# Kernel tuning notes

Measured on AMD Instinct MI355X. Metric: run time of the kernel, lower is better.

Reference implementation:

```python
import jax, jax.numpy as jnp
import numpy as np

# TT config (matches init_kwargs)
NUM_TABLES = 4
P = (100, 100, 100)          # tt_p_shapes, prod = num_embeddings = 1e6
Q = (4, 4, 4)                # tt_q_shapes, prod = embedding_dim = 64
R = (1, 32, 32, 1)           # tt_ranks with boundary ranks
BAGS_PER_TABLE = 8192
POOL = 16                    # indices per bag


def setup_inputs() -> dict:
    key = jax.random.key(0)
    k1, k2, k3, k4 = jax.random.split(key, 4)
    nnz = NUM_TABLES * BAGS_PER_TABLE * POOL      # 524288
    B = NUM_TABLES * BAGS_PER_TABLE               # 32768 bags total
    indices = jax.random.randint(k1, (nnz,), 0, P[0] * P[1] * P[2], dtype=jnp.int64)
    offsets = (jnp.arange(B + 1, dtype=jnp.int64) * POOL)
    scale = 0.05  # small init, akin to approx-normal weight_dist
    tt_core_0 = jax.random.normal(k2, (NUM_TABLES, P[0], R[0] * Q[0] * R[1]), dtype=jnp.float32) * scale
    tt_core_1 = jax.random.normal(k3, (NUM_TABLES, P[1], R[1] * Q[1] * R[2]), dtype=jnp.float32) * scale
    tt_core_2 = jax.random.normal(k4, (NUM_TABLES, P[2], R[2] * Q[2] * R[3]), dtype=jnp.float32) * scale
    return {"indices": indices, "offsets": offsets,
            "tt_core_0": tt_core_0, "tt_core_1": tt_core_1, "tt_core_2": tt_core_2}


def reference(indices, offsets, tt_core_0, tt_core_1, tt_core_2):
    nnz = indices.shape[0]
    B = offsets.shape[0] - 1
    bags_per_table = B // NUM_TABLES

    # bag id for each nonzero (embedding-bag semantics), then table id per nonzero
    rowidx = jnp.searchsorted(offsets, jnp.arange(nnz, dtype=offsets.dtype), side='right') - 1
    tableidx = rowidx // bags_per_table

    # decompose flat row index into TT indices (C-order over p-shapes,
    # matching tt_matrix_to_full row layout)
    i0 = indices // (P[1] * P[2])
    i1 = (indices // P[2]) % P[1]
    i2 = indices % P[2]

    # gather per-lookup core slices
    c0 = tt_core_0[tableidx, i0].reshape(nnz, Q[0], R[1])          # r0 == 1
    c1 = tt_core_1[tableidx, i1].reshape(nnz, R[1], Q[1], R[2])
    c2 = tt_core_2[tableidx, i2].reshape(nnz, R[2], Q[2])          # r3 == 1

    # on-the-fly TT contraction to reconstruct embedding rows [nnz, D]
    t = jnp.einsum('nar,nrbs->nabs', c0, c1)                       # [nnz, q0, q1, r2]
    rows = jnp.einsum('nabs,nsc->nabc', t, c2).reshape(nnz, Q[0] * Q[1] * Q[2])

    # sum-pool per bag
    out = jax.ops.segment_sum(rows, rowidx, num_segments=B)        # [B, D]
    return out
```

## Files before the change

### kernel.cpp

```cpp
#include <hip/hip_runtime.h>
#include <stdint.h>

#define NT 4
#define PP 100
#define TT_BYTES (4ull * 100 * 100 * 1024)
#define C2B_DWORDS (NT * PP * 64)


typedef short bf16x8 __attribute__((ext_vector_type(8)));
typedef float f32x4  __attribute__((ext_vector_type(4)));

__device__ __forceinline__ uint32_t f2bf(float f) {
    union { float f; uint32_t u; } v; v.f = f;
    uint32_t u = v.u;
    return (u + 0x7fffu + ((u >> 16) & 1u)) >> 16;
}

__global__ __launch_bounds__(256)
void tt_phase1(const float* __restrict__ c0g, const float* __restrict__ c1g,
               unsigned short* __restrict__ tT,
               const float* __restrict__ c2g, uint32_t* __restrict__ c2p) {
    __shared__ uint32_t       A_l[112 * 16];
    __shared__ uint32_t       B_l[128 * 16];
    __shared__ unsigned short D_l[100 * 128];

    int blk = blockIdx.x;
    int tid = threadIdx.x;

    if (blk >= 1600) {
        int t = (blk - 1600) * 256 + tid;
        if (t < C2B_DWORDS) {
            int sg = t & 15, c = (t >> 4) & 3, combo = t >> 6;
            const float* src = c2g + (size_t)combo * 128;
            c2p[t] = f2bf(src[(2 * sg) * 4 + c]) | (f2bf(src[(2 * sg + 1) * 4 + c]) << 16);
        }
        return;
    }

    int tab = blk / 400;
    int rem = blk % 400;
    int i1  = rem >> 2;
    int ch  = rem & 3;

    if (tid < 192) A_l[1600 + tid] = 0u;

    const float2* a2 = (const float2*)(c0g + (size_t)tab * 12800 + (size_t)ch * 3200);
    #pragma unroll
    for (int it = 0; it < 7; ++it) {
        int d = tid + it * 256;
        if (d < 1600) {
            float2 v = a2[d];
            int row = d >> 4, kd = d & 15;
            A_l[row * 16 + (kd ^ ((row & 3) << 2))] = f2bf(v.x) | (f2bf(v.y) << 16);
        }
    }
    const float* c1row = c1g + ((size_t)tab * PP + i1) * 4096;
    #pragma unroll
    for (int it = 0; it < 8; ++it) {
        int j = tid + it * 256;
        int n = j & 127, rp = j >> 7;
        float e = c1row[(2 * rp) * 128 + n];
        float o = c1row[(2 * rp + 1) * 128 + n];
        B_l[n * 16 + (rp ^ ((n & 3) << 2))] = f2bf(e) | (f2bf(o) << 16);
    }
    __syncthreads();

    int lane = tid & 63, wv = tid >> 6;
    int col = lane & 15, kq = lane >> 4;

    #pragma unroll
    for (int mt = 0; mt < 7; ++mt) {
        #pragma unroll
        for (int ntl = 0; ntl < 2; ++ntl) {
            int nt = wv * 2 + ntl;
            int arow = mt * 16 + col;
            int bn   = nt * 16 + col;
            bf16x8 af = *(const bf16x8*)&A_l[arow * 16 + ((kq ^ (arow & 3)) << 2)];
            bf16x8 bf = *(const bf16x8*)&B_l[bn   * 16 + ((kq ^ (bn   & 3)) << 2)];
            f32x4 acc = {0.f, 0.f, 0.f, 0.f};
            acc = __builtin_amdgcn_mfma_f32_16x16x32_bf16(af, bf, acc, 0, 0, 0);
            #pragma unroll
            for (int q = 0; q < 4; ++q) {
                int Drow = mt * 16 + kq * 4 + q;
                if (Drow < 100)
                    D_l[Drow * 128 + nt * 16 + col] = (unsigned short)f2bf(acc[q]);
            }
        }
    }
    __syncthreads();

    #pragma unroll
    for (int it = 0; it < 7; ++it) {
        int c = tid + it * 256;
        if (c < 1600) {
            int Drow = c >> 4, w = c & 15;
            int i0l = Drow >> 2, a = Drow & 3;
            int b = w >> 2, so = w & 3;
            int i0 = ch * 25 + i0l;
            size_t combo = (size_t)tab * 10000 + (size_t)i0 * 100 + (size_t)i1;
            char* dst = (char*)tT + combo * 1024 + (size_t)(a * 4 + b) * 64 + (size_t)so * 16;
            *(uint4*)dst = *(const uint4*)&D_l[Drow * 128 + w * 8];
        }
    }
}

__global__ __launch_bounds__(256, 6)
void tt_phase2(const int* __restrict__ indices, const int* __restrict__ offsets,
               const char* __restrict__ tT, const char* __restrict__ c2b,
               float* __restrict__ out, int bags_per_table, int B) {
    __shared__ float red[4][64];
    int lane = threadIdx.x & 63;
    int wv   = threadIdx.x >> 6;
    int bag  = blockIdx.x;
    int col = lane & 15;
    int kq  = lane >> 4;
    int tab = bag / bags_per_table;
    int start = offsets[bag];

    uint32_t idx = (uint32_t)indices[start + wv * 4 + (col & 3)];
    uint32_t i0 = idx / 10000u;
    uint32_t r1 = idx - i0 * 10000u;
    uint32_t i1 = r1 / 100u;
    uint32_t i2 = r1 - i1 * 100u;
    uint32_t tby = (((uint32_t)tab * 10000u + i0 * 100u + i1) << 10);
    uint32_t cby = (((uint32_t)tab * 100u + i2) << 8);

    int aoff = col * 64 + kq * 16;
    int boff = (col & 3) * 64 + kq * 16;

    bf16x8 A[4], Bv[4];
    #pragma unroll
    for (int jj = 0; jj < 4; ++jj) {
        uint32_t tb = (uint32_t)__builtin_amdgcn_readlane((int)tby, jj);
        uint32_t cb = (uint32_t)__builtin_amdgcn_readlane((int)cby, jj);
        A[jj]  = *(const bf16x8*)(tT  + tb + aoff);
        Bv[jj] = *(const bf16x8*)(c2b + cb + boff);
    }

    f32x4 acc = {0.f, 0.f, 0.f, 0.f};
    #pragma unroll
    for (int jj = 0; jj < 4; ++jj)
        acc = __builtin_amdgcn_mfma_f32_16x16x32_bf16(A[jj], Bv[jj], acc, 0, 0, 0);

    if (col < 4) {
        #pragma unroll
        for (int q = 0; q < 4; ++q)
            red[wv][kq * 16 + q * 4 + col] = acc[q];
    }
    __syncthreads();
    if (wv == 0) {
        float s = red[0][lane] + red[1][lane] + red[2][lane] + red[3][lane];
        out[(size_t)bag * 64 + lane] = s;
    }
}

extern "C" void kernel_launch(void* const* d_in, const int* in_sizes, int n_in,
                              void* d_out, int out_size, void* d_ws, size_t ws_size,
                              hipStream_t stream) {
    const int*   indices = (const int*)d_in[0];
    const int*   offsets = (const int*)d_in[1];
    const float* c0      = (const float*)d_in[2];
    const float* c1      = (const float*)d_in[3];
    const float* c2      = (const float*)d_in[4];
    float* out = (float*)d_out;

    int B = in_sizes[1] - 1;
    int bags_per_table = B / NT;

    unsigned short* tT  = (unsigned short*)d_ws;
    uint32_t*       c2p = (uint32_t*)((char*)d_ws + TT_BYTES);

    tt_phase1<<<dim3(1700), dim3(256), 0, stream>>>(c0, c1, tT, c2, c2p);
    tt_phase2<<<dim3(B), dim3(256), 0, stream>>>(indices, offsets,
                                                 (const char*)tT,
                                                 (const char*)c2p, out,
                                                 bags_per_table, B);
}
```

Before: 144.2 us.

## Fuse both phases into one persistent cooperative kernel with a grid sync

Merges the TT-core precompute and the per-bag lookup kernels into one persistent cooperative kernel. Blocks grid-stride over the phase-1 work, meet at a grid-wide barrier, then grid-stride over the bags. The aim is to drop the second kernel launch and the gap between kernels. In exchange, the grid is capped by occupancy, which now reflects the larger phase-1 shared-memory footprint and no longer carries phase2's launch bound of 6, so phase 2 may run with fewer concurrent bags and pays a grid-sync cost.

```diff
diff --git a/kernel.cpp b/kernel.cpp
--- a/kernel.cpp
+++ b/kernel.cpp
@@ -1,5 +1,8 @@
 #include <hip/hip_runtime.h>
+#include <hip/hip_cooperative_groups.h>
 #include <stdint.h>
+
+namespace cg = cooperative_groups;
 
 #define NT 4
 #define PP 100
@@ -17,140 +20,140 @@
 }
 
 __global__ __launch_bounds__(256)
-void tt_phase1(const float* __restrict__ c0g, const float* __restrict__ c1g,
-               unsigned short* __restrict__ tT,
-               const float* __restrict__ c2g, uint32_t* __restrict__ c2p) {
+void tt_fused(const float* __restrict__ c0g, const float* __restrict__ c1g,
+              unsigned short* __restrict__ tT,
+              const float* __restrict__ c2g, uint32_t* __restrict__ c2p,
+              const int* __restrict__ indices, const int* __restrict__ offsets,
+              float* __restrict__ out, int bags_per_table, int B) {
     __shared__ uint32_t       A_l[112 * 16];
     __shared__ uint32_t       B_l[128 * 16];
     __shared__ unsigned short D_l[100 * 128];
 
-    int blk = blockIdx.x;
-    int tid = threadIdx.x;
+    int tid  = threadIdx.x;
+    int lane = tid & 63, wv = tid >> 6;
+    int col  = lane & 15, kq = lane >> 4;
 
-    if (blk >= 1600) {
-        int t = (blk - 1600) * 256 + tid;
-        if (t < C2B_DWORDS) {
-            int sg = t & 15, c = (t >> 4) & 3, combo = t >> 6;
-            const float* src = c2g + (size_t)combo * 128;
-            c2p[t] = f2bf(src[(2 * sg) * 4 + c]) | (f2bf(src[(2 * sg + 1) * 4 + c]) << 16);
+    for (int blk = blockIdx.x; blk < 1700; blk += gridDim.x) {
+        if (blk >= 1600) {
+            int t = (blk - 1600) * 256 + tid;
+            if (t < C2B_DWORDS) {
+                int sg = t & 15, c = (t >> 4) & 3, combo = t >> 6;
+                const float* src = c2g + (size_t)combo * 128;
+                c2p[t] = f2bf(src[(2 * sg) * 4 + c]) |
+                         (f2bf(src[(2 * sg + 1) * 4 + c]) << 16);
+            }
+        } else {
+            int tab = blk / 400;
+            int rem = blk % 400;
+            int i1  = rem >> 2;
+            int ch  = rem & 3;
+
+            if (tid < 192) A_l[1600 + tid] = 0u;
+
+            const float2* a2 = (const float2*)(c0g + (size_t)tab * 12800 + (size_t)ch * 3200);
+            #pragma unroll
+            for (int it = 0; it < 7; ++it) {
+                int d = tid + it * 256;
+                if (d < 1600) {
+                    float2 v = a2[d];
+                    int row = d >> 4, kd = d & 15;
+                    A_l[row * 16 + (kd ^ ((row & 3) << 2))] = f2bf(v.x) | (f2bf(v.y) << 16);
+                }
+            }
+            const float* c1row = c1g + ((size_t)tab * PP + i1) * 4096;
+            #pragma unroll
+            for (int it = 0; it < 8; ++it) {
+                int j = tid + it * 256;
+                int n = j & 127, rp = j >> 7;
+                float e = c1row[(2 * rp) * 128 + n];
+                float o = c1row[(2 * rp + 1) * 128 + n];
+                B_l[n * 16 + (rp ^ ((n & 3) << 2))] = f2bf(e) | (f2bf(o) << 16);
+            }
+            __syncthreads();
+
+            #pragma unroll
+            for (int mt = 0; mt < 7; ++mt) {
+                #pragma unroll
+                for (int ntl = 0; ntl < 2; ++ntl) {
+                    int nt = wv * 2 + ntl;
+                    int arow = mt * 16 + col;
+                    int bn   = nt * 16 + col;
+                    bf16x8 af = *(const bf16x8*)&A_l[arow * 16 + ((kq ^ (arow & 3)) << 2)];
+                    bf16x8 bf = *(const bf16x8*)&B_l[bn   * 16 + ((kq ^ (bn   & 3)) << 2)];
+                    f32x4 acc = {0.f, 0.f, 0.f, 0.f};
+                    acc = __builtin_amdgcn_mfma_f32_16x16x32_bf16(af, bf, acc, 0, 0, 0);
+                    #pragma unroll
+                    for (int q = 0; q < 4; ++q) {
+                        int Drow = mt * 16 + kq * 4 + q;
+                        if (Drow < 100)
+                            D_l[Drow * 128 + nt * 16 + col] = (unsigned short)f2bf(acc[q]);
+                    }
+                }
+            }
+            __syncthreads();
+
+            #pragma unroll
+            for (int it = 0; it < 7; ++it) {
+                int c = tid + it * 256;
+                if (c < 1600) {
+                    int Drow = c >> 4, w = c & 15;
+                    int i0l = Drow >> 2, a = Drow & 3;
+                    int b = w >> 2, so = w & 3;
+                    int i0 = ch * 25 + i0l;
+                    size_t combo = (size_t)tab * 10000 + (size_t)i0 * 100 + (size_t)i1;
+                    char* dst = (char*)tT + combo * 1024 + (size_t)(a * 4 + b) * 64 + (size_t)so * 16;
+                    *(uint4*)dst = *(const uint4*)&D_l[Drow * 128 + w * 8];
+                }
+            }
         }
-        return;
+        __syncthreads();
     }
 
-    int tab = blk / 400;
-    int rem = blk % 400;
-    int i1  = rem >> 2;
-    int ch  = rem & 3;
+    cg::this_grid().sync();
 
-    if (tid < 192) A_l[1600 + tid] = 0u;
-
-    const float2* a2 = (const float2*)(c0g + (size_t)tab * 12800 + (size_t)ch * 3200);
-    #pragma unroll
-    for (int it = 0; it < 7; ++it) {
-        int d = tid + it * 256;
-        if (d < 1600) {
-            float2 v = a2[d];
-            int row = d >> 4, kd = d & 15;
-            A_l[row * 16 + (kd ^ ((row & 3) << 2))] = f2bf(v.x) | (f2bf(v.y) << 16);
-        }
-    }
-    const float* c1row = c1g + ((size_t)tab * PP + i1) * 4096;
-    #pragma unroll
-    for (int it = 0; it < 8; ++it) {
-        int j = tid + it * 256;
-        int n = j & 127, rp = j >> 7;
-        float e = c1row[(2 * rp) * 128 + n];
-        float o = c1row[(2 * rp + 1) * 128 + n];
-        B_l[n * 16 + (rp ^ ((n & 3) << 2))] = f2bf(e) | (f2bf(o) << 16);
-    }
-    __syncthreads();
-
-    int lane = tid & 63, wv = tid >> 6;
-    int col = lane & 15, kq = lane >> 4;
-
-    #pragma unroll
-    for (int mt = 0; mt < 7; ++mt) {
-        #pragma unroll
-        for (int ntl = 0; ntl < 2; ++ntl) {
-            int nt = wv * 2 + ntl;
-            int arow = mt * 16 + col;
-            int bn   = nt * 16 + col;
-            bf16x8 af = *(const bf16x8*)&A_l[arow * 16 + ((kq ^ (arow & 3)) << 2)];
-            bf16x8 bf = *(const bf16x8*)&B_l[bn   * 16 + ((kq ^ (bn   & 3)) << 2)];
-            f32x4 acc = {0.f, 0.f, 0.f, 0.f};
-            acc = __builtin_amdgcn_mfma_f32_16x16x32_bf16(af, bf, acc, 0, 0, 0);
-            #pragma unroll
-            for (int q = 0; q < 4; ++q) {
-                int Drow = mt * 16 + kq * 4 + q;
-                if (Drow < 100)
-                    D_l[Drow * 128 + nt * 16 + col] = (unsigned short)f2bf(acc[q]);
-            }
-        }
-    }
-    __syncthreads();
-
-    #pragma unroll
-    for (int it = 0; it < 7; ++it) {
-        int c = tid + it * 256;
-        if (c < 1600) {
-            int Drow = c >> 4, w = c & 15;
-            int i0l = Drow >> 2, a = Drow & 3;
-            int b = w >> 2, so = w & 3;
-            int i0 = ch * 25 + i0l;
-            size_t combo = (size_t)tab * 10000 + (size_t)i0 * 100 + (size_t)i1;
-            char* dst = (char*)tT + combo * 1024 + (size_t)(a * 4 + b) * 64 + (size_t)so * 16;
-            *(uint4*)dst = *(const uint4*)&D_l[Drow * 128 + w * 8];
-        }
-    }
-}
-
-__global__ __launch_bounds__(256, 6)
-void tt_phase2(const int* __restrict__ indices, const int* __restrict__ offsets,
-               const char* __restrict__ tT, const char* __restrict__ c2b,
-               float* __restrict__ out, int bags_per_table, int B) {
-    __shared__ float red[4][64];
-    int lane = threadIdx.x & 63;
-    int wv   = threadIdx.x >> 6;
-    int bag  = blockIdx.x;
-    int col = lane & 15;
-    int kq  = lane >> 4;
-    int tab = bag / bags_per_table;
-    int start = offsets[bag];
-
-    uint32_t idx = (uint32_t)indices[start + wv * 4 + (col & 3)];
-    uint32_t i0 = idx / 10000u;
-    uint32_t r1 = idx - i0 * 10000u;
-    uint32_t i1 = r1 / 100u;
-    uint32_t i2 = r1 - i1 * 100u;
-    uint32_t tby = (((uint32_t)tab * 10000u + i0 * 100u + i1) << 10);
-    uint32_t cby = (((uint32_t)tab * 100u + i2) << 8);
-
+    float* red = (float*)D_l;
     int aoff = col * 64 + kq * 16;
     int boff = (col & 3) * 64 + kq * 16;
+    const char* tTb = (const char*)tT;
+    const char* c2b = (const char*)c2p;
 
-    bf16x8 A[4], Bv[4];
-    #pragma unroll
-    for (int jj = 0; jj < 4; ++jj) {
-        uint32_t tb = (uint32_t)__builtin_amdgcn_readlane((int)tby, jj);
-        uint32_t cb = (uint32_t)__builtin_amdgcn_readlane((int)cby, jj);
-        A[jj]  = *(const bf16x8*)(tT  + tb + aoff);
-        Bv[jj] = *(const bf16x8*)(c2b + cb + boff);
-    }
+    for (int bag = blockIdx.x; bag < B; bag += gridDim.x) {
+        int tab = bag / bags_per_table;
+        int start = offsets[bag];
 
-    f32x4 acc = {0.f, 0.f, 0.f, 0.f};
-    #pragma unroll
-    for (int jj = 0; jj < 4; ++jj)
-        acc = __builtin_amdgcn_mfma_f32_16x16x32_bf16(A[jj], Bv[jj], acc, 0, 0, 0);
+        uint32_t idx = (uint32_t)indices[start + wv * 4 + (col & 3)];
+        uint32_t i0 = idx / 10000u;
+        uint32_t r1 = idx - i0 * 10000u;
+        uint32_t i1 = r1 / 100u;
+        uint32_t i2 = r1 - i1 * 100u;
+        uint32_t tby = (((uint32_t)tab * 10000u + i0 * 100u + i1) << 10);
+        uint32_t cby = (((uint32_t)tab * 100u + i2) << 8);
 
-    if (col < 4) {
+        bf16x8 A[4], Bv[4];
         #pragma unroll
-        for (int q = 0; q < 4; ++q)
-            red[wv][kq * 16 + q * 4 + col] = acc[q];
-    }
-    __syncthreads();
-    if (wv == 0) {
-        float s = red[0][lane] + red[1][lane] + red[2][lane] + red[3][lane];
-        out[(size_t)bag * 64 + lane] = s;
+        for (int jj = 0; jj < 4; ++jj) {
+            uint32_t tb = (uint32_t)__builtin_amdgcn_readlane((int)tby, jj);
+            uint32_t cb = (uint32_t)__builtin_amdgcn_readlane((int)cby, jj);
+            A[jj]  = *(const bf16x8*)(tTb + tb + aoff);
+            Bv[jj] = *(const bf16x8*)(c2b + cb + boff);
+        }
+
+        f32x4 acc = {0.f, 0.f, 0.f, 0.f};
+        #pragma unroll
+        for (int jj = 0; jj < 4; ++jj)
+            acc = __builtin_amdgcn_mfma_f32_16x16x32_bf16(A[jj], Bv[jj], acc, 0, 0, 0);
+
+        if (col < 4) {
+            #pragma unroll
+            for (int q = 0; q < 4; ++q)
+                red[wv * 64 + kq * 16 + q * 4 + col] = acc[q];
+        }
+        __syncthreads();
+        if (wv == 0) {
+            float s = red[lane] + red[64 + lane] + red[128 + lane] + red[192 + lane];
+            out[(size_t)bag * 64 + lane] = s;
+        }
+        __syncthreads();
     }
 }
 
@@ -170,9 +173,17 @@
     unsigned short* tT  = (unsigned short*)d_ws;
     uint32_t*       c2p = (uint32_t*)((char*)d_ws + TT_BYTES);
 
-    tt_phase1<<<dim3(1700), dim3(256), 0, stream>>>(c0, c1, tT, c2, c2p);
-    tt_phase2<<<dim3(B), dim3(256), 0, stream>>>(indices, offsets,
-                                                 (const char*)tT,
-                                                 (const char*)c2p, out,
-                                                 bags_per_table, B);
+    static int maxb = -1;
+    if (maxb < 0) {
+        (void)hipOccupancyMaxActiveBlocksPerMultiprocessor(&maxb, tt_fused, 256, 0);
+        if (maxb < 1) maxb = 1;
+    }
+    int grid = maxb * 256;
+    if (grid > B) grid = B;
+
+    void* args[] = { (void*)&c0, (void*)&c1, (void*)&tT, (void*)&c2, (void*)&c2p,
+                     (void*)&indices, (void*)&offsets, (void*)&out,
+                     (void*)&bags_per_table, (void*)&B };
+    (void)hipLaunchCooperativeKernel((void*)tt_fused, dim3(grid), dim3(256),
+                                     args, 0, stream);
 }
```

Result: slower. 285.9 us (+98.3%).
